# Optimization experiments

Hardware: AMD Instinct MI355X
Metric: run time of the kernel (lower is better)

## Reference

```python
import jax, jax.numpy as jnp
import numpy as np

N_NODES = 100000
N_EDGES = 1600000
D = 32


def setup_inputs() -> dict:
    key = jax.random.key(0)
    k1, k2, k3, k4, k5, k6, k7 = jax.random.split(key, 7)
    x = jax.random.normal(k1, (N_NODES, D), dtype=jnp.float32)
    edge_index = jax.random.randint(k2, (2, N_EDGES), 0, N_NODES, dtype=jnp.int64)
    edge_weight = jax.random.uniform(k3, (N_EDGES,), dtype=jnp.float32)
    s = 1.0 / np.sqrt(D)
    W1 = jax.random.uniform(k4, (D, D), jnp.float32, -s, s)
    b1 = jax.random.uniform(k5, (D,), jnp.float32, -s, s)
    W2 = jax.random.uniform(k6, (D, D), jnp.float32, -s, s)
    b2 = jax.random.uniform(k7, (D,), jnp.float32, -s, s)
    return {"x": x, "edge_index": edge_index, "edge_weight": edge_weight,
            "W1": W1, "b1": b1, "W2": W2, "b2": b2}


def reference(x, edge_index, edge_weight, W1, b1, W2, b2):
    N = x.shape[0]
    src, dst = edge_index[0], edge_index[1]
    # gcn_norm with improved=True: self-loops get fill value 2.0
    loops = jnp.arange(N, dtype=edge_index.dtype)
    src_a = jnp.concatenate([src, loops])
    dst_a = jnp.concatenate([dst, loops])
    w_a = jnp.concatenate([edge_weight, jnp.full((N,), 2.0, x.dtype)])
    deg = jax.ops.segment_sum(w_a, dst_a, num_segments=N)          # [N]
    dinv = jnp.where(deg > 0, jax.lax.rsqrt(deg), 0.0)             # deg^-1/2, inf->0
    norm = dinv[src_a] * w_a * dinv[dst_a]                          # [E+N]

    def gcn_conv(h, W, b):
        h = h @ W                                                   # [N,D] dense transform
        msg = h[src_a] * norm[:, None]                              # gather + normalize [E+N,D]
        return jax.ops.segment_sum(msg, dst_a, num_segments=N) + b  # scatter-add + bias

    h = jax.nn.relu(gcn_conv(x, W1, b1))
    h = jax.nn.relu(gcn_conv(h, W2, b2))
    # F.dropout treated as identity (deterministic inference reference)
    return h
```

## Files before the change

### kernel.cpp

```cpp
#include <hip/hip_runtime.h>

#define D       32
#define BS      256
#define CBLK    500
#define MAXBUCK 2048
#define MAX_EPT 13
#define ECAP    4096
#define POISON_BASE ((int)0xAAAAAAAAu)

__device__ inline unsigned bf16pack2(float a, float b) {
    unsigned ua = __float_as_uint(a);
    unsigned ub = __float_as_uint(b);
    ua = (ua + 0x7FFFu + ((ua >> 16) & 1)) >> 16;
    ub = (ub + 0x7FFFu + ((ub >> 16) & 1)) >> 16;
    return ua | (ub << 16);
}
__device__ inline uint2 bf16pack4(float4 v) {
    return make_uint2(bf16pack2(v.x, v.y), bf16pack2(v.z, v.w));
}
__device__ inline float4 bf16unpack4(uint2 h) {
    return make_float4(__uint_as_float(h.x << 16),
                       __uint_as_float(h.x & 0xFFFF0000u),
                       __uint_as_float(h.y << 16),
                       __uint_as_float(h.y & 0xFFFF0000u));
}

__global__ void k_localsort_gemm(const int* __restrict__ dst, const int* __restrict__ src,
                                 const float* __restrict__ w, int* __restrict__ bc,
                                 int* __restrict__ locoff, int2* __restrict__ staged,
                                 int E, int EPB, int NBUCK,
                                 const float* __restrict__ X, const float* __restrict__ Wm,
                                 uint2* __restrict__ H, int n) {
    __shared__ int    bins[MAXBUCK];
    __shared__ int    sscan[BS];
    __shared__ int    carry;
    __shared__ float4 Ws[D * 8];
    int t = threadIdx.x;

    if ((int)blockIdx.x >= CBLK) {
        for (int i = t; i < D * 8; i += BS) Ws[i] = ((const float4*)Wm)[i];
        __syncthreads();
        int gid  = (blockIdx.x - CBLK) * BS + t;
        int node = gid >> 3;
        int q    = gid & 7;
        if (node >= n) return;
        float4 xv  = ((const float4*)X)[node * 8 + q];
        float4 acc = make_float4(0.f, 0.f, 0.f, 0.f);
#pragma unroll
        for (int k = 0; k < D; ++k) {
            float comp = (k & 3) == 0 ? xv.x : (k & 3) == 1 ? xv.y
                       : (k & 3) == 2 ? xv.z : xv.w;
            float  xk = __shfl(comp, k >> 2, 8);
            float4 wr = Ws[k * 8 + q];
            acc.x += xk * wr.x; acc.y += xk * wr.y;
            acc.z += xk * wr.z; acc.w += xk * wr.w;
        }
        H[node * 8 + q] = bf16pack4(acc);
        return;
    }

    int blk = blockIdx.x;
    int beg = blk * EPB;
    int end = min(E, beg + EPB);
    for (int i = t; i < NBUCK; i += BS) bins[i] = 0;
    __syncthreads();

    int stash[MAX_EPT];
#pragma unroll
    for (int i = 0; i < MAX_EPT; ++i) {
        int e = beg + i * BS + t;
        stash[i] = -1;
        if (e < end) {
            int dv = dst[e];
            int b  = dv >> 6;
            int r  = atomicAdd(&bins[b], 1);
            stash[i] = (b << 19) | ((dv & 63) << 13) | r;
        }
    }
    __syncthreads();
    for (int i = t; i < NBUCK; i += BS) bc[i * CBLK + blk] = bins[i];
    __syncthreads();
    if (t == 0) carry = 0;
    __syncthreads();
    for (int base = 0; base < NBUCK; base += BS) {
        int idx = base + t;
        int v = (idx < NBUCK) ? bins[idx] : 0;
        sscan[t] = v;
        __syncthreads();
        for (int off = 1; off < BS; off <<= 1) {
            int u = (t >= off) ? sscan[t - off] : 0;
            __syncthreads();
            sscan[t] += u;
            __syncthreads();
        }
        if (idx < NBUCK) bins[idx] = carry + sscan[t] - v;
        __syncthreads();
        if (t == 0) carry += sscan[BS - 1];
        __syncthreads();
    }
    for (int i = t; i < NBUCK; i += BS) locoff[i * CBLK + blk] = bins[i];
    __syncthreads();

    int2* myslice = staged + (size_t)blk * EPB;
#pragma unroll
    for (int i = 0; i < MAX_EPT; ++i) {
        if (stash[i] >= 0) {
            int e     = beg + i * BS + t;
            int b     = stash[i] >> 19;
            int local = (stash[i] >> 13) & 63;
            int r     = stash[i] & 0x1FFF;
            int pos   = bins[b] + r;
            myslice[pos] = make_int2(src[e] | (local << 17), __float_as_int(w[e]));
        }
    }
}

__global__ void k_scanA(const int* __restrict__ bc, int* __restrict__ asum, int m) {
    __shared__ int s[BS];
    int t = threadIdx.x, i = blockIdx.x * BS + t;
    s[t] = (i < m) ? bc[i] : 0;
    __syncthreads();
    for (int off = BS / 2; off > 0; off >>= 1) {
        if (t < off) s[t] += s[t + off];
        __syncthreads();
    }
    if (t == 0) asum[blockIdx.x] = s[0];
}

__global__ void k_scanB(const int* __restrict__ asum, int* __restrict__ aex, int m) {
    __shared__ int s[BS];
    __shared__ int carry;
    int t = threadIdx.x;
    if (t == 0) carry = 0;
    __syncthreads();
    for (int base = 0; base < m; base += BS) {
        int i = base + t;
        int v = (i < m) ? asum[i] : 0;
        s[t] = v;
        __syncthreads();
        for (int off = 1; off < BS; off <<= 1) {
            int u = (t >= off) ? s[t - off] : 0;
            __syncthreads();
            s[t] += u;
            __syncthreads();
        }
        if (i < m) aex[i] = carry + s[t] - v;
        __syncthreads();
        if (t == BS - 1) carry += s[BS - 1];
        __syncthreads();
    }
}

__global__ void k_scanC(int* __restrict__ bc, const int* __restrict__ aex, int m) {
    __shared__ int s[BS];
    int t = threadIdx.x, i = blockIdx.x * BS + t;
    int v = (i < m) ? bc[i] : 0;
    s[t] = v;
    __syncthreads();
    for (int off = 1; off < BS; off <<= 1) {
        int u = (t >= off) ? s[t - off] : 0;
        __syncthreads();
        s[t] += u;
        __syncthreads();
    }
    if (i < m) bc[i] = aex[blockIdx.x] + s[t] - v;
}

__global__ void k_merge(const int* __restrict__ sc, const int* __restrict__ locoff,
                        const int2* __restrict__ staged, int2* __restrict__ emeta,
                        int* __restrict__ rowptr, float* __restrict__ dinv,
                        int N, int E, int NBUCK, int EPB, int M) {
    __shared__ int2  ebuf[ECAP];
    __shared__ int   ihist[64];
    __shared__ float fdeg[64];
    __shared__ int   cursor[64];
    __shared__ int   fitsf;
    int b = blockIdx.x, t = threadIdx.x;
    int bstart = sc[b * CBLK];
    int bend   = (b == NBUCK - 1) ? E : sc[(b + 1) * CBLK];
    if (t < 64) { ihist[t] = 0; fdeg[t] = 0.0f; }
    if (t == 0) fitsf = (bend - bstart) <= ECAP;
    __syncthreads();
    bool fits = fitsf;

    for (int rr = t; rr < CBLK; rr += BS) {
        int cell = b * CBLK + rr;
        int gs = sc[cell];
        int ge = (cell + 1 < M) ? sc[cell + 1] : E;
        int ls = locoff[cell];
        const int2* run = staged + (size_t)rr * EPB + ls;
        for (int j = 0; j < ge - gs; ++j) {
            int2 v = run[j];
            int local = (v.x >> 17) & 63;
            atomicAdd(&ihist[local], 1);
            atomicAdd(&fdeg[local], __int_as_float(v.y));
            if (fits) ebuf[gs - bstart + j] = v;
        }
    }
    __syncthreads();
    if (t < 64) {
        int v = ihist[t];
        int incl = v;
#pragma unroll
        for (int off = 1; off < 64; off <<= 1) {
            int u = __shfl_up(incl, off, 64);
            if (t >= off) incl += u;
        }
        int excl = incl - v;
        int node = b * 64 + t;
        if (node < N) {
            rowptr[node] = bstart + excl;
            dinv[node]   = rsqrtf(2.0f + fdeg[t]);
        }
        if (b == NBUCK - 1 && t == 0) rowptr[N] = E;
        cursor[t] = excl;
    }
    __syncthreads();
    for (int rr = t; rr < CBLK; rr += BS) {
        int cell = b * CBLK + rr;
        int gs = sc[cell];
        int ge = (cell + 1 < M) ? sc[cell + 1] : E;
        int ls = locoff[cell];
        const int2* run = staged + (size_t)rr * EPB + ls;
        for (int j = 0; j < ge - gs; ++j) {
            int2 v = fits ? ebuf[gs - bstart + j] : run[j];
            int local = (v.x >> 17) & 63;
            int r = atomicAdd(&cursor[local], 1);
            emeta[bstart + r] = make_int2(v.x & 0x1FFFF, v.y);
        }
    }
}


__global__ void k_gemm(const float* __restrict__ X, const float* __restrict__ W,
                       uint2* __restrict__ H, int n) {
    __shared__ float4 Ws[D * 8];
    int tid = threadIdx.x;
    for (int i = tid; i < D * 8; i += blockDim.x) Ws[i] = ((const float4*)W)[i];
    __syncthreads();
    int gid  = blockIdx.x * blockDim.x + tid;
    int node = gid >> 3;
    int q    = gid & 7;
    if (node >= n) return;
    float4 xv  = ((const float4*)X)[node * 8 + q];
    float4 acc = make_float4(0.f, 0.f, 0.f, 0.f);
#pragma unroll
    for (int k = 0; k < D; ++k) {
        float comp = (k & 3) == 0 ? xv.x : (k & 3) == 1 ? xv.y
                   : (k & 3) == 2 ? xv.z : xv.w;
        float  xk = __shfl(comp, k >> 2, 8);
        float4 wr = Ws[k * 8 + q];
        acc.x += xk * wr.x; acc.y += xk * wr.y;
        acc.z += xk * wr.z; acc.w += xk * wr.w;
    }
    H[node * 8 + q] = bf16pack4(acc);
}

template <bool NORM_STORE, bool FUSE_GEMM>
__global__ void k_aggregate(const int* __restrict__ rowptr, int2* __restrict__ emeta,
                            const uint2* __restrict__ H, const float* __restrict__ dinv,
                            const float* __restrict__ b, const float* __restrict__ W2,
                            void* __restrict__ outv, int n) {
    __shared__ float4 Ws[D * 8];
    int tid = threadIdx.x;
    if (FUSE_GEMM) {
        for (int i = tid; i < D * 8; i += BS) Ws[i] = ((const float4*)W2)[i];
        __syncthreads();
    }

    int gid  = blockIdx.x * BS + tid;
    int node = gid >> 3;
    int q    = gid & 7;
    if (node >= n) return;

    float  di = dinv[node];
    float  s2 = 2.0f * di * di;
    float4 bq = ((const float4*)b)[q];
    float4 h0 = bf16unpack4(H[node * 8 + q]);
    float4 acc = make_float4(h0.x * s2 + bq.x, h0.y * s2 + bq.y,
                             h0.z * s2 + bq.z, h0.w * s2 + bq.w);

    int beg  = rowptr[node];
    int end  = rowptr[node + 1];
    int full = beg + ((end - beg) & ~7);

    for (int i0 = beg; i0 < full; i0 += 8) {
        int  idx = i0 + q;
        int2 em  = emeta[idx];
        float nm;
        if (NORM_STORE) {
            nm = dinv[em.x] * __int_as_float(em.y) * di;
            emeta[idx].y = __float_as_int(nm);
        } else {
            nm = __int_as_float(em.y);
        }
#pragma unroll
        for (int j = 0; j < 8; ++j) {
            int    s   = __shfl(em.x, j, 8);
            float  nmj = __shfl(nm, j, 8);
            float4 hv  = bf16unpack4(H[s * 8 + q]);
            acc.x += nmj * hv.x; acc.y += nmj * hv.y;
            acc.z += nmj * hv.z; acc.w += nmj * hv.w;
        }
    }
    if (full < end) {
        int  idx = full + q;
        bool ok  = idx < end;
        int2 em  = ok ? emeta[idx] : make_int2(0, 0);
        float nm;
        if (NORM_STORE) {
            nm = ok ? dinv[em.x] * __int_as_float(em.y) * di : 0.0f;
            if (ok) emeta[idx].y = __float_as_int(nm);
        } else {
            nm = __int_as_float(em.y);
        }
        int rem = end - full;
        for (int j = 0; j < rem; ++j) {
            int    s   = __shfl(em.x, j, 8);
            float  nmj = __shfl(nm, j, 8);
            float4 hv  = bf16unpack4(H[s * 8 + q]);
            acc.x += nmj * hv.x; acc.y += nmj * hv.y;
            acc.z += nmj * hv.z; acc.w += nmj * hv.w;
        }
    }
    acc.x = fmaxf(acc.x, 0.f); acc.y = fmaxf(acc.y, 0.f);
    acc.z = fmaxf(acc.z, 0.f); acc.w = fmaxf(acc.w, 0.f);

    if (FUSE_GEMM) {
        float4 o = make_float4(0.f, 0.f, 0.f, 0.f);
#pragma unroll
        for (int k = 0; k < D; ++k) {
            float comp = (k & 3) == 0 ? acc.x : (k & 3) == 1 ? acc.y
                       : (k & 3) == 2 ? acc.z : acc.w;
            float  hk = __shfl(comp, k >> 2, 8);
            float4 wr = Ws[k * 8 + q];
            o.x += hk * wr.x; o.y += hk * wr.y;
            o.z += hk * wr.z; o.w += hk * wr.w;
        }
        ((uint2*)outv)[node * 8 + q] = bf16pack4(o);
    } else {
        ((float4*)outv)[node * 8 + q] = acc;
    }
}

__global__ void k_hist_gemm(const int4* __restrict__ dst4, int* __restrict__ cnt,
                            int4* __restrict__ rank4, int E4,
                            const float* __restrict__ X, const float* __restrict__ W,
                            uint2* __restrict__ H, int n, int gE4) {
    __shared__ float4 Ws[D * 8];
    int tid = threadIdx.x;
    if ((int)blockIdx.x < gE4) {
        int i = blockIdx.x * BS + tid;
        if (i >= E4) return;
        int4 d = dst4[i];
        int4 r;
        r.x = atomicAdd(&cnt[d.x], 1) - POISON_BASE;
        r.y = atomicAdd(&cnt[d.y], 1) - POISON_BASE;
        r.z = atomicAdd(&cnt[d.z], 1) - POISON_BASE;
        r.w = atomicAdd(&cnt[d.w], 1) - POISON_BASE;
        rank4[i] = r;
        return;
    }
    for (int i = tid; i < D * 8; i += BS) Ws[i] = ((const float4*)W)[i];
    __syncthreads();
    int gid  = (blockIdx.x - gE4) * BS + tid;
    int node = gid >> 3;
    int q    = gid & 7;
    if (node >= n) return;
    float4 xv  = ((const float4*)X)[node * 8 + q];
    float4 acc = make_float4(0.f, 0.f, 0.f, 0.f);
#pragma unroll
    for (int k = 0; k < D; ++k) {
        float comp = (k & 3) == 0 ? xv.x : (k & 3) == 1 ? xv.y
                   : (k & 3) == 2 ? xv.z : xv.w;
        float  xk = __shfl(comp, k >> 2, 8);
        float4 wr = Ws[k * 8 + q];
        acc.x += xk * wr.x; acc.y += xk * wr.y;
        acc.z += xk * wr.z; acc.w += xk * wr.w;
    }
    H[node * 8 + q] = bf16pack4(acc);
}

__global__ void k_scan1(const int* __restrict__ cnt, int* __restrict__ bsum, int n) {
    __shared__ int s[BS];
    int t = threadIdx.x, i = blockIdx.x * BS + t;
    s[t] = (i < n) ? (cnt[i] - POISON_BASE) : 0;
    __syncthreads();
    for (int off = BS / 2; off > 0; off >>= 1) {
        if (t < off) s[t] += s[t + off];
        __syncthreads();
    }
    if (t == 0) bsum[blockIdx.x] = s[0];
}

__global__ void k_scan23(const int* __restrict__ cnt, const int* __restrict__ bsum,
                         int* __restrict__ rowptr, int n) {
    __shared__ int red[BS];
    __shared__ int s[BS];
    int t = threadIdx.x, i = blockIdx.x * BS + t;
    int pacc = 0;
    for (int k = t; k < (int)blockIdx.x; k += BS) pacc += bsum[k];
    red[t] = pacc;
    __syncthreads();
    for (int off = BS / 2; off > 0; off >>= 1) {
        if (t < off) red[t] += red[t + off];
        __syncthreads();
    }
    int bpre = red[0];
    int v = (i < n) ? (cnt[i] - POISON_BASE) : 0;
    s[t] = v;
    __syncthreads();
    for (int off = 1; off < BS; off <<= 1) {
        int u = (t >= off) ? s[t - off] : 0;
        __syncthreads();
        s[t] += u;
        __syncthreads();
    }
    if (i < n) {
        int excl = bpre + s[t] - v;
        rowptr[i] = excl;
        if (i == n - 1) rowptr[n] = excl + v;
    }
}

__global__ void k_reorder(const int4* __restrict__ src4, const int4* __restrict__ dst4,
                          const float4* __restrict__ w4, const int4* __restrict__ rank4,
                          const int* __restrict__ rowptr, int2* __restrict__ emeta, int E4) {
    int i = blockIdx.x * blockDim.x + threadIdx.x;
    if (i >= E4) return;
    int4   s = src4[i];
    int4   d = dst4[i];
    float4 w = w4[i];
    int4   r = rank4[i];
    emeta[rowptr[d.x] + r.x] = make_int2(s.x, __float_as_int(w.x));
    emeta[rowptr[d.y] + r.y] = make_int2(s.y, __float_as_int(w.y));
    emeta[rowptr[d.z] + r.z] = make_int2(s.z, __float_as_int(w.z));
    emeta[rowptr[d.w] + r.w] = make_int2(s.w, __float_as_int(w.w));
}

__global__ void k_degF(const int* __restrict__ rowptr, const int2* __restrict__ emeta,
                       float* __restrict__ dinv, int n) {
    int gid  = blockIdx.x * blockDim.x + threadIdx.x;
    int node = gid >> 3;
    int c    = gid & 7;
    if (node >= n) return;
    int beg = rowptr[node], end = rowptr[node + 1];
    float sum = 0.0f;
    for (int idx = beg + c; idx < end; idx += 8)
        sum += __int_as_float(emeta[idx].y);
    sum += __shfl_xor(sum, 4, 8);
    sum += __shfl_xor(sum, 2, 8);
    sum += __shfl_xor(sum, 1, 8);
    if (c == 0) dinv[node] = rsqrtf(2.0f + sum);
}

extern "C" void kernel_launch(void* const* d_in, const int* in_sizes, int n_in,
                              void* d_out, int out_size, void* d_ws, size_t ws_size,
                              hipStream_t stream) {
    const float* x   = (const float*)d_in[0];
    const int*   ei  = (const int*)d_in[1];
    const float* w   = (const float*)d_in[2];
    const float* W1  = (const float*)d_in[3];
    const float* b1  = (const float*)d_in[4];
    const float* W2  = (const float*)d_in[5];
    const float* b2  = (const float*)d_in[6];
    float*       out = (float*)d_out;

    const int N = in_sizes[0] / D;
    const int E = in_sizes[2];
    const int* src = ei;
    const int* dst = ei + E;

    const int NBUCK = (N + 63) / 64;
    const int EPB   = (E + CBLK - 1) / CBLK;
    const int M     = NBUCK * CBLK;
    const int MA    = (M + BS - 1) / BS;
    const int NB    = (N + BS - 1) / BS;
    const int E4    = E / 4;
    const int gE4   = (E4 + BS - 1) / BS;
    const int gN8   = (N * 8 + BS - 1) / BS;

    char*  base   = (char*)d_ws;
    int2*  emeta  = (int2*)base;
    uint2* ht     = (uint2*)(base + (size_t)E * 8);
    uint2* ht2    = ht + (size_t)N * 8;
    float* dinv   = (float*)(ht2 + (size_t)N * 8);
    int*   rowptr = (int*)(dinv + N);
    int2*  staged = (int2*)(rowptr + ((N + 4) & ~3));
    int*   bc     = (int*)(staged + E);
    int*   locoff = bc + ((M + 3) & ~3);
    int*   asum   = locoff + ((M + 3) & ~3);
    int*   aex    = asum + ((MA + 3) & ~3);
    size_t need   = (size_t)((char*)(aex + MA) - base);

    bool main_ok = (ws_size >= need) && (NBUCK <= MAXBUCK) && (N < (1 << 17)) &&
                   ((EPB + BS - 1) / BS <= MAX_EPT) && (EPB <= 8192) && (N % 4 == 0);

    if (main_ok) {
        k_localsort_gemm<<<CBLK + gN8, BS, 0, stream>>>(dst, src, w, bc, locoff, staged,
                                                        E, EPB, NBUCK, x, W1, ht, N);
        k_scanA<<<MA, BS, 0, stream>>>(bc, asum, M);
        k_scanB<<<1, BS, 0, stream>>>(asum, aex, MA);
        k_scanC<<<MA, BS, 0, stream>>>(bc, aex, M);
        k_merge<<<NBUCK, BS, 0, stream>>>(bc, locoff, staged, emeta, rowptr, dinv,
                                          N, E, NBUCK, EPB, M);
        k_aggregate<true,  true ><<<gN8, BS, 0, stream>>>(rowptr, emeta, ht,  dinv, b1, W2, ht2, N);
        k_aggregate<false, false><<<gN8, BS, 0, stream>>>(rowptr, emeta, ht2, dinv, b2, nullptr, out, N);
    } else {
        int* cnt  = (int*)staged;
        int* rank = cnt + N;
        int* bsum = rank + E;
        k_hist_gemm<<<gE4 + gN8, BS, 0, stream>>>((const int4*)dst, cnt, (int4*)rank, E4,
                                                  x, W1, ht, N, gE4);
        k_scan1 <<<NB, BS, 0, stream>>>(cnt, bsum, N);
        k_scan23<<<NB, BS, 0, stream>>>(cnt, bsum, rowptr, N);
        k_reorder<<<(E4 + BS - 1) / BS, BS, 0, stream>>>((const int4*)src, (const int4*)dst,
                                                         (const float4*)w, (const int4*)rank,
                                                         rowptr, emeta, E4);
        k_degF<<<gN8, BS, 0, stream>>>(rowptr, emeta, dinv, N);
        k_aggregate<true,  false><<<gN8, BS, 0, stream>>>(rowptr, emeta, ht, dinv, b1, nullptr, out, N);
        k_gemm<<<gN8, BS, 0, stream>>>(out, W2, ht, N);
        k_aggregate<false, false><<<gN8, BS, 0, stream>>>(rowptr, emeta, ht, dinv, b2, nullptr, out, N);
    }
}
```

Before: 225.9 us.

## Transpose bucket-count layout and replace global three-pass scan with per-bucket scans

```diff
diff --git a/kernel.cpp b/kernel.cpp
--- a/kernel.cpp
+++ b/kernel.cpp
@@ -28,7 +28,7 @@
 __global__ void k_localsort_gemm(const int* __restrict__ dst, const int* __restrict__ src,
                                  const float* __restrict__ w, int* __restrict__ bc,
                                  int* __restrict__ locoff, int2* __restrict__ staged,
-                                 int E, int EPB, int NBUCK,
+                                 int E, int EPB, int NBUCK, int NBUCKP,
                                  const float* __restrict__ X, const float* __restrict__ Wm,
                                  uint2* __restrict__ H, int n) {
     __shared__ int    bins[MAXBUCK];
@@ -78,7 +78,7 @@
         }
     }
     __syncthreads();
-    for (int i = t; i < NBUCK; i += BS) bc[i * CBLK + blk] = bins[i];
+    for (int i = t; i < NBUCK; i += BS) bc[blk * NBUCKP + i] = bins[i];
     __syncthreads();
     if (t == 0) carry = 0;
     __syncthreads();
@@ -98,7 +98,7 @@
         if (t == 0) carry += sscan[BS - 1];
         __syncthreads();
     }
-    for (int i = t; i < NBUCK; i += BS) locoff[i * CBLK + blk] = bins[i];
+    for (int i = t; i < NBUCK; i += BS) locoff[blk * NBUCKP + i] = bins[i];
     __syncthreads();
 
     int2* myslice = staged + (size_t)blk * EPB;
@@ -115,16 +115,13 @@
     }
 }
 
-__global__ void k_scanA(const int* __restrict__ bc, int* __restrict__ asum, int m) {
-    __shared__ int s[BS];
-    int t = threadIdx.x, i = blockIdx.x * BS + t;
-    s[t] = (i < m) ? bc[i] : 0;
-    __syncthreads();
-    for (int off = BS / 2; off > 0; off >>= 1) {
-        if (t < off) s[t] += s[t + off];
-        __syncthreads();
-    }
-    if (t == 0) asum[blockIdx.x] = s[0];
+__global__ void k_btot(const int* __restrict__ bc, int* __restrict__ btot,
+                       int NBUCK, int NBUCKP) {
+    int b = blockIdx.x * BS + threadIdx.x;
+    if (b >= NBUCK) return;
+    int s = 0;
+    for (int k = 0; k < CBLK; ++k) s += bc[k * NBUCKP + b];
+    btot[b] = s;
 }
 
 __global__ void k_scanB(const int* __restrict__ asum, int* __restrict__ aex, int m) {
@@ -151,50 +148,54 @@
     }
 }
 
-__global__ void k_scanC(int* __restrict__ bc, const int* __restrict__ aex, int m) {
-    __shared__ int s[BS];
-    int t = threadIdx.x, i = blockIdx.x * BS + t;
-    int v = (i < m) ? bc[i] : 0;
-    s[t] = v;
-    __syncthreads();
-    for (int off = 1; off < BS; off <<= 1) {
-        int u = (t >= off) ? s[t - off] : 0;
-        __syncthreads();
-        s[t] += u;
-        __syncthreads();
-    }
-    if (i < m) bc[i] = aex[blockIdx.x] + s[t] - v;
-}
-
-__global__ void k_merge(const int* __restrict__ sc, const int* __restrict__ locoff,
-                        const int2* __restrict__ staged, int2* __restrict__ emeta,
-                        int* __restrict__ rowptr, float* __restrict__ dinv,
-                        int N, int E, int NBUCK, int EPB, int M) {
+__global__ void k_merge(const int* __restrict__ bc, const int* __restrict__ locoff,
+                        const int* __restrict__ boff, const int2* __restrict__ staged,
+                        int2* __restrict__ emeta, int* __restrict__ rowptr,
+                        float* __restrict__ dinv, int N, int E, int NBUCK, int NBUCKP,
+                        int EPB) {
     __shared__ int2  ebuf[ECAP];
+    __shared__ int   runoff[CBLK];
+    __shared__ int   sscan[BS];
+    __shared__ int   carry;
     __shared__ int   ihist[64];
     __shared__ float fdeg[64];
     __shared__ int   cursor[64];
-    __shared__ int   fitsf;
     int b = blockIdx.x, t = threadIdx.x;
-    int bstart = sc[b * CBLK];
-    int bend   = (b == NBUCK - 1) ? E : sc[(b + 1) * CBLK];
+
+    for (int k = t; k < CBLK; k += BS) runoff[k] = bc[k * NBUCKP + b];
     if (t < 64) { ihist[t] = 0; fdeg[t] = 0.0f; }
-    if (t == 0) fitsf = (bend - bstart) <= ECAP;
-    __syncthreads();
-    bool fits = fitsf;
-
-    for (int rr = t; rr < CBLK; rr += BS) {
-        int cell = b * CBLK + rr;
-        int gs = sc[cell];
-        int ge = (cell + 1 < M) ? sc[cell + 1] : E;
-        int ls = locoff[cell];
-        const int2* run = staged + (size_t)rr * EPB + ls;
+    if (t == 0) carry = 0;
+    __syncthreads();
+    for (int base = 0; base < CBLK; base += BS) {
+        int idx = base + t;
+        int v = (idx < CBLK) ? runoff[idx] : 0;
+        sscan[t] = v;
+        __syncthreads();
+        for (int off = 1; off < BS; off <<= 1) {
+            int u = (t >= off) ? sscan[t - off] : 0;
+            __syncthreads();
+            sscan[t] += u;
+            __syncthreads();
+        }
+        if (idx < CBLK) runoff[idx] = carry + sscan[t] - v;
+        __syncthreads();
+        if (t == 0) carry += sscan[BS - 1];
+        __syncthreads();
+    }
+    int total  = carry;
+    int bstart = boff[b];
+    bool fits  = total <= ECAP;
+
+    for (int k = t; k < CBLK; k += BS) {
+        int gs = runoff[k];
+        int ge = (k + 1 < CBLK) ? runoff[k + 1] : total;
+        const int2* run = staged + (size_t)k * EPB + locoff[k * NBUCKP + b];
         for (int j = 0; j < ge - gs; ++j) {
             int2 v = run[j];
             int local = (v.x >> 17) & 63;
             atomicAdd(&ihist[local], 1);
             atomicAdd(&fdeg[local], __int_as_float(v.y));
-            if (fits) ebuf[gs - bstart + j] = v;
+            if (fits) ebuf[gs + j] = v;
         }
     }
     __syncthreads();
@@ -216,14 +217,12 @@
         cursor[t] = excl;
     }
     __syncthreads();
-    for (int rr = t; rr < CBLK; rr += BS) {
-        int cell = b * CBLK + rr;
-        int gs = sc[cell];
-        int ge = (cell + 1 < M) ? sc[cell + 1] : E;
-        int ls = locoff[cell];
-        const int2* run = staged + (size_t)rr * EPB + ls;
+    for (int k = t; k < CBLK; k += BS) {
+        int gs = runoff[k];
+        int ge = (k + 1 < CBLK) ? runoff[k + 1] : total;
+        const int2* run = staged + (size_t)k * EPB + locoff[k * NBUCKP + b];
         for (int j = 0; j < ge - gs; ++j) {
-            int2 v = fits ? ebuf[gs - bstart + j] : run[j];
+            int2 v = fits ? ebuf[gs + j] : run[j];
             int local = (v.x >> 17) & 63;
             int r = atomicAdd(&cursor[local], 1);
             emeta[bstart + r] = make_int2(v.x & 0x1FFFF, v.y);
@@ -471,14 +470,13 @@
     const int* src = ei;
     const int* dst = ei + E;
 
-    const int NBUCK = (N + 63) / 64;
-    const int EPB   = (E + CBLK - 1) / CBLK;
-    const int M     = NBUCK * CBLK;
-    const int MA    = (M + BS - 1) / BS;
-    const int NB    = (N + BS - 1) / BS;
-    const int E4    = E / 4;
-    const int gE4   = (E4 + BS - 1) / BS;
-    const int gN8   = (N * 8 + BS - 1) / BS;
+    const int NBUCK  = (N + 63) / 64;
+    const int NBUCKP = (NBUCK + 3) & ~3;
+    const int EPB    = (E + CBLK - 1) / CBLK;
+    const int NB     = (N + BS - 1) / BS;
+    const int E4     = E / 4;
+    const int gE4    = (E4 + BS - 1) / BS;
+    const int gN8    = (N * 8 + BS - 1) / BS;
 
     char*  base   = (char*)d_ws;
     int2*  emeta  = (int2*)base;
@@ -488,22 +486,21 @@
     int*   rowptr = (int*)(dinv + N);
     int2*  staged = (int2*)(rowptr + ((N + 4) & ~3));
     int*   bc     = (int*)(staged + E);
-    int*   locoff = bc + ((M + 3) & ~3);
-    int*   asum   = locoff + ((M + 3) & ~3);
-    int*   aex    = asum + ((MA + 3) & ~3);
-    size_t need   = (size_t)((char*)(aex + MA) - base);
+    int*   locoff = bc + (size_t)CBLK * NBUCKP;
+    int*   btot   = locoff + (size_t)CBLK * NBUCKP;
+    int*   boff   = btot + NBUCKP;
+    size_t need   = (size_t)((char*)(boff + NBUCKP) - base);
 
     bool main_ok = (ws_size >= need) && (NBUCK <= MAXBUCK) && (N < (1 << 17)) &&
                    ((EPB + BS - 1) / BS <= MAX_EPT) && (EPB <= 8192) && (N % 4 == 0);
 
     if (main_ok) {
         k_localsort_gemm<<<CBLK + gN8, BS, 0, stream>>>(dst, src, w, bc, locoff, staged,
-                                                        E, EPB, NBUCK, x, W1, ht, N);
-        k_scanA<<<MA, BS, 0, stream>>>(bc, asum, M);
-        k_scanB<<<1, BS, 0, stream>>>(asum, aex, MA);
-        k_scanC<<<MA, BS, 0, stream>>>(bc, aex, M);
-        k_merge<<<NBUCK, BS, 0, stream>>>(bc, locoff, staged, emeta, rowptr, dinv,
-                                          N, E, NBUCK, EPB, M);
+                                                        E, EPB, NBUCK, NBUCKP, x, W1, ht, N);
+        k_btot <<<(NBUCK + BS - 1) / BS, BS, 0, stream>>>(bc, btot, NBUCK, NBUCKP);
+        k_scanB<<<1, BS, 0, stream>>>(btot, boff, NBUCK);
+        k_merge<<<NBUCK, BS, 0, stream>>>(bc, locoff, boff, staged, emeta, rowptr, dinv,
+                                          N, E, NBUCK, NBUCKP, EPB);
         k_aggregate<true,  true ><<<gN8, BS, 0, stream>>>(rowptr, emeta, ht,  dinv, b1, W2, ht2, N);
         k_aggregate<false, false><<<gN8, BS, 0, stream>>>(rowptr, emeta, ht2, dinv, b2, nullptr, out, N);
     } else {
@@ -520,6 +517,6 @@
         k_degF<<<gN8, BS, 0, stream>>>(rowptr, emeta, dinv, N);
         k_aggregate<true,  false><<<gN8, BS, 0, stream>>>(rowptr, emeta, ht, dinv, b1, nullptr, out, N);
         k_gemm<<<gN8, BS, 0, stream>>>(out, W2, ht, N);
-        k_aggregate<false, false><<<gN8, BS, 0, stream>>>(rowptr, emeta, ht, dinv, b2, nullptr, out, N);
-    }
-}
+        k_aggregate<false, false><<<gN8, BS, 0, stream>>>(rowptr, emeta, ht2, dinv, b2, nullptr, out, N);
+    }
+}
```

Measured after the change: 239.3 us. 1.06x slower.
